# Kernel optimization log

Measured on AMD Instinct MI355X. Metric: run time of the kernel, lower is better.

## Reference

```python
import jax, jax.numpy as jnp
import numpy as np

# Problem sizes (see shape_source)
N_MICRO, E_MICRO = 131072, 1048576
N_MACRO, E_MACRO = 6400, 51200
B, T, NG = 64, 50, 5          # batch graphs, target_seq_len, nodes_per_group
IN_DIM, H, S = 384, 256, 64   # in_dim, hidden_dim, state_dim
NODES_PER_MACRO = 100         # N_MACRO // B


def gcn_conv(x, ei, ew, W, b, num_nodes):
    """PyG-style GCNConv with self-loops: out = D^-1/2 (A+I) D^-1/2 (xW) + b."""
    h = x @ W                                     # [N, H]
    src, dst = ei[0], ei[1]
    deg = jax.ops.segment_sum(ew, dst, num_segments=num_nodes) + 1.0  # +1 self loop
    dinv = jax.lax.rsqrt(deg)
    norm = dinv[src] * ew * dinv[dst]             # [E]
    out = jax.ops.segment_sum(h[src] * norm[:, None], dst, num_segments=num_nodes)
    out = out + h * (dinv * dinv)[:, None]        # self-loop term
    return out + b


def mamba_block(u, W_in, W_dtBC, dt_bias, A_log, Dp, W_out):
    """Mamba2-style selective scan block with gating and residual. u: [B, T, H]."""
    Bb, Tt, Hh = u.shape
    xz = u @ W_in                                  # [B,T,2H]
    x, z = xz[..., :Hh], xz[..., Hh:]
    dbc = u @ W_dtBC                               # [B,T,1+2S]
    n = (dbc.shape[-1] - 1) // 2
    dt = jax.nn.softplus(dbc[..., :1] + dt_bias)   # [B,T,1]
    Bm = dbc[..., 1:1 + n]                         # [B,T,S]
    Cm = dbc[..., 1 + n:]                          # [B,T,S]
    A = -jnp.exp(A_log)                            # [H]
    decay = jnp.exp(dt * A)                        # [B,T,H]
    dx = dt * x                                    # [B,T,H]

    def step(hst, inp):
        dec_t, dx_t, b_t, c_t = inp                # [B,H],[B,H],[B,S],[B,S]
        hst = dec_t[:, :, None] * hst + dx_t[:, :, None] * b_t[:, None, :]
        y_t = jnp.einsum('bhn,bn->bh', hst, c_t)
        return hst, y_t

    h0 = jnp.zeros((Bb, Hh, n), dtype=u.dtype)
    inputs = (decay.transpose(1, 0, 2), dx.transpose(1, 0, 2),
              Bm.transpose(1, 0, 2), Cm.transpose(1, 0, 2))
    _, ys = jax.lax.scan(step, h0, inputs)         # ys: [T,B,H]
    y = ys.transpose(1, 0, 2) + Dp * x
    return (y * jax.nn.silu(z)) @ W_out + u


def setup_inputs() -> dict:
    key = jax.random.key(0)
    ks = jax.random.split(key, 16)
    sc = 0.02
    d = {}
    d['micro_x'] = jax.random.normal(ks[0], (N_MICRO, IN_DIM), jnp.float32)
    d['micro_ew'] = jax.random.uniform(ks[1], (E_MICRO,), jnp.float32)
    d['macro_x'] = jax.random.normal(ks[2], (N_MACRO, IN_DIM), jnp.float32)
    d['macro_ew'] = jax.random.uniform(ks[3], (E_MACRO,), jnp.float32)
    d['Wg_micro'] = jax.random.normal(ks[4], (IN_DIM, H), jnp.float32) * sc
    d['bg_micro'] = jnp.zeros((H,), jnp.float32)
    d['Wg_macro'] = jax.random.normal(ks[5], (IN_DIM, H), jnp.float32) * sc
    d['bg_macro'] = jnp.zeros((H,), jnp.float32)
    d['W_in'] = jax.random.normal(ks[6], (H, 2 * H), jnp.float32) * sc
    d['W_dtBC'] = jax.random.normal(ks[7], (H, 1 + 2 * S), jnp.float32) * sc
    d['dt_bias'] = jnp.zeros((1,), jnp.float32)
    d['A_log'] = jnp.zeros((H,), jnp.float32)
    d['Dp'] = jnp.ones((H,), jnp.float32)
    d['W_out'] = jax.random.normal(ks[8], (H, H), jnp.float32) * sc
    d['W1'] = jax.random.normal(ks[9], (2 * H, H), jnp.float32) * sc
    d['b1'] = jnp.zeros((H,), jnp.float32)
    d['W2'] = jax.random.normal(ks[10], (H, 2 * H), jnp.float32) * sc
    d['b2'] = jnp.zeros((2 * H,), jnp.float32)
    d['micro_ei'] = jax.random.randint(ks[11], (2, E_MICRO), 0, N_MICRO, jnp.int32)
    d['gather_idx'] = jax.random.randint(ks[12], (B, T, NG), 0, N_MICRO, jnp.int32)
    d['mask'] = jnp.ones((B, T), jnp.bool_)
    d['macro_ei'] = jax.random.randint(ks[13], (2, E_MACRO), 0, N_MACRO, jnp.int32)
    return d


def reference(micro_x, micro_ew, macro_x, macro_ew, Wg_micro, bg_micro,
              Wg_macro, bg_macro, W_in, W_dtBC, dt_bias, A_log, Dp, W_out,
              W1, b1, W2, b2, micro_ei, gather_idx, mask, macro_ei):
    # micro branch: per-snapshot GCN over the flattened batched snapshot graph
    gcn_out = gcn_conv(micro_x, micro_ei, micro_ew, Wg_micro, bg_micro, N_MICRO)
    # scatter GCN outputs into padded [B,T,NG,H] embeddings, zero where masked
    emb = gcn_out[gather_idx] * mask[:, :, None, None].astype(gcn_out.dtype)
    seq = emb.mean(axis=2)                          # [B,T,H] mean over node slots
    seq = mamba_block(seq, W_in, W_dtBC, dt_bias, A_log, Dp, W_out)
    micro_pooled = seq[:, -1]                       # [B,H]
    # macro branch: GCN + per-graph mean pooling (fixed nodes per graph)
    macro_feat = gcn_conv(macro_x, macro_ei, macro_ew, Wg_macro, bg_macro, N_MACRO)
    macro_pooled = macro_feat.reshape(B, NODES_PER_MACRO, H).mean(axis=1)
    pooled = jnp.concatenate([macro_pooled, micro_pooled], axis=-1)  # [B,2H]
    return jax.nn.relu(pooled @ W1 + b1) @ W2 + b2   # [B,2H]
```

## Files before the change

### kernel.cpp

```cpp
#include <hip/hip_runtime.h>
#include <hip/hip_bf16.h>
#include <cstdint>

#define NMICRO 131072
#define EMICRO 1048576
#define NMACRO 6400
#define EMACRO 51200
#define BB 64
#define TT 50
#define NGATH 5
#define INDIM 384
#define HDIM 256
#define SDIM 64
#define NPM 100
#define NGIDX (BB*TT*NGATH)
#define NINBC 641

typedef __bf16 bf16x8 __attribute__((ext_vector_type(8)));
typedef float  f32x4  __attribute__((ext_vector_type(4)));

#define WT_E0 (INDIM*HDIM)
#define WT_E1 (WT_E0 + 512*HDIM)
#define WT_E2 (WT_E1 + 129*HDIM)
__global__ __launch_bounds__(256) void k_setup(float* __restrict__ degm, float* __restrict__ dega,
                                               int* __restrict__ slot, int* __restrict__ cntm,
                                               int* __restrict__ cnta, int* __restrict__ counters,
                                               const float* __restrict__ Wg, __bf16* __restrict__ Tg,
                                               const float* __restrict__ Win, const float* __restrict__ Wdbc,
                                               __bf16* __restrict__ Tinbc) {
    int i = blockIdx.x * 256 + threadIdx.x;
    if (i < NMICRO) { degm[i] = 1.0f; slot[i] = -1; }
    if (i < NMACRO) { dega[i] = 1.0f; cnta[i] = 0; }
    if (i < NGIDX)  cntm[i] = 0;
    if (i < 64)     counters[i] = 0;
    if (i < WT_E0) {
        int nn = i / INDIM, kk = i - nn * INDIM;
        Tg[i] = (__bf16)Wg[(size_t)kk * HDIM + nn];
    } else if (i < WT_E1) {
        int j = i - WT_E0;
        int nn = j / HDIM, kk = j - nn * HDIM;
        Tinbc[j] = (__bf16)Win[(size_t)kk * 512 + nn];
    } else if (i < WT_E2) {
        int j = i - WT_E1;
        int nn = j / HDIM, kk = j - nn * HDIM;
        Tinbc[(size_t)512 * HDIM + j] = (__bf16)Wdbc[(size_t)kk * 129 + nn];
    }
}

__global__ void k_slot(const int* __restrict__ gidx, int* __restrict__ slot,
                       int* __restrict__ counter, int* __restrict__ node_of_slot) {
    int i = blockIdx.x * 256 + threadIdx.x;
    if (i >= NGIDX) return;
    int node = gidx[i];
    if (atomicCAS(&slot[node], -1, -2) == -1) {
        int s = atomicAdd(counter, 1);
        node_of_slot[s] = node;
        slot[node] = s;
    }
}

__global__ __launch_bounds__(256) void k_deg_count(const int* __restrict__ mei, const float* __restrict__ mew,
                                                   float* __restrict__ degm, const int* __restrict__ slot,
                                                   int* __restrict__ cntm,
                                                   const int* __restrict__ aei, const float* __restrict__ aew,
                                                   float* __restrict__ dega, int* __restrict__ cnta) {
    int i = blockIdx.x * 256 + threadIdx.x;
    if (i >= EMICRO + EMACRO) return;
    if (i < EMICRO) {
        int dst = mei[EMICRO + i];
        atomicAdd(&degm[dst], mew[i]);
        int s = slot[dst];
        if (s >= 0) atomicAdd(&cntm[s], 1);
    } else {
        int j = i - EMICRO;
        int dst = aei[EMACRO + j];
        atomicAdd(&dega[dst], aew[j]);
        atomicAdd(&cnta[dst], 1);
    }
}

__global__ __launch_bounds__(1024) void k_scan_rsqrt(const int* __restrict__ cm, int* __restrict__ sm, int* __restrict__ um,
                                                     const int* __restrict__ ca, int* __restrict__ sa, int* __restrict__ ua,
                                                     float* __restrict__ degm, float* __restrict__ dega) {
    if (blockIdx.x >= 2) {
        int i = (blockIdx.x - 2) * 1024 + threadIdx.x;
        if (i < NMICRO) degm[i] = rsqrtf(degm[i]);
        else { int j = i - NMICRO; if (j < NMACRO) dega[j] = rsqrtf(dega[j]); }
        return;
    }
    const int* cnt; int* start; int* cursor; int n;
    if (blockIdx.x == 0) { cnt = cm; start = sm; cursor = um; n = NGIDX; }
    else                 { cnt = ca; start = sa; cursor = ua; n = NMACRO; }
    __shared__ int wsum[16];
    __shared__ int carry_s;
    const int tid = threadIdx.x;
    const int lane = tid & 63, wv = tid >> 6;
    if (tid == 0) carry_s = 0;
    __syncthreads();
    for (int base = 0; base < n; base += 1024) {
        int i = base + tid;
        int v = (i < n) ? cnt[i] : 0;
        int x = v;
#pragma unroll
        for (int off = 1; off < 64; off <<= 1) {
            int y = __shfl_up(x, off, 64);
            if (lane >= off) x += y;
        }
        if (lane == 63) wsum[wv] = x;
        __syncthreads();
        int carry = carry_s;
        if (wv == 0) {
            int s = (lane < 16) ? wsum[lane] : 0;
#pragma unroll
            for (int off = 1; off < 16; off <<= 1) {
                int y = __shfl_up(s, off, 64);
                if (lane >= off) s += y;
            }
            if (lane < 16) wsum[lane] = s;
        }
        __syncthreads();
        int woff = (wv == 0) ? 0 : wsum[wv - 1];
        if (i < n) { int e = carry + woff + x - v; start[i] = e; cursor[i] = e; }
        __syncthreads();
        if (tid == 0) carry_s = carry + wsum[15];
    }
}

__global__ __launch_bounds__(256) void k_fillcsr(const int* __restrict__ mei, const float* __restrict__ mew,
                                                 const int* __restrict__ slot, const float* __restrict__ dinvm,
                                                 int* __restrict__ curm, int* __restrict__ csrm_src, float* __restrict__ csrm_nrm,
                                                 const int* __restrict__ aei, const float* __restrict__ aew,
                                                 const float* __restrict__ dinva,
                                                 int* __restrict__ cura, int* __restrict__ csra_src, float* __restrict__ csra_nrm) {
    int i = blockIdx.x * 256 + threadIdx.x;
    if (i >= EMICRO + EMACRO) return;
    if (i < EMICRO) {
        int dst = mei[EMICRO + i];
        int s = slot[dst];
        if (s >= 0) {
            int src = mei[i];
            int p = atomicAdd(&curm[s], 1);
            csrm_src[p] = src;
            csrm_nrm[p] = dinvm[src] * mew[i] * dinvm[dst];
        }
    } else {
        int j = i - EMICRO;
        int dst = aei[EMACRO + j];
        int src = aei[j];
        int p = atomicAdd(&cura[dst], 1);
        csra_src[p] = src;
        csra_nrm[p] = dinva[src] * aew[j] * dinva[dst];
    }
}

__global__ __launch_bounds__(256) void k_agg_both(const int* __restrict__ node_of_slot, const int* __restrict__ nslots,
                                                  const int* __restrict__ startm, const int* __restrict__ cntm,
                                                  const int* __restrict__ csrm_src, const float* __restrict__ csrm_nrm,
                                                  const float* __restrict__ xm, const float* __restrict__ dinvm,
                                                  float* __restrict__ aggm,
                                                  const int* __restrict__ starta, const int* __restrict__ cnta,
                                                  const int* __restrict__ csra_src, const float* __restrict__ csra_nrm,
                                                  const float* __restrict__ xa, const float* __restrict__ dinva,
                                                  float* __restrict__ agga) {
    int gwid = (blockIdx.x * 256 + threadIdx.x) >> 6;
    int lane = threadIdx.x & 63;
    if (gwid < NGIDX) {
        if (gwid >= nslots[0]) return;
        int node = node_of_slot[gwid];
        float di = dinvm[node];
        float sc = di * di;
        const float* xr = xm + (size_t)node * INDIM;
        float4 a0 = ((const float4*)xr)[lane];
        float2 a1 = ((const float2*)(xr + 256))[lane];
        a0.x *= sc; a0.y *= sc; a0.z *= sc; a0.w *= sc; a1.x *= sc; a1.y *= sc;
        int st = startm[gwid], en = st + cntm[gwid];
        for (int e = st; e < en; e++) {
            int src = csrm_src[e]; float nrm = csrm_nrm[e];
            const float* r = xm + (size_t)src * INDIM;
            float4 v0 = ((const float4*)r)[lane];
            float2 v1 = ((const float2*)(r + 256))[lane];
            a0.x += v0.x * nrm; a0.y += v0.y * nrm; a0.z += v0.z * nrm; a0.w += v0.w * nrm;
            a1.x += v1.x * nrm; a1.y += v1.y * nrm;
        }
        float* o = aggm + (size_t)gwid * INDIM;
        ((float4*)o)[lane] = a0;
        ((float2*)(o + 256))[lane] = a1;
    } else {
        int wid = gwid - NGIDX;
        if (wid >= NMACRO) return;
        float di = dinva[wid];
        float sc = di * di;
        const float* xr = xa + (size_t)wid * INDIM;
        float4 a0 = ((const float4*)xr)[lane];
        float2 a1 = ((const float2*)(xr + 256))[lane];
        a0.x *= sc; a0.y *= sc; a0.z *= sc; a0.w *= sc; a1.x *= sc; a1.y *= sc;
        int st = starta[wid], en = st + cnta[wid];
        for (int e = st; e < en; e++) {
            int src = csra_src[e]; float nrm = csra_nrm[e];
            const float* r = xa + (size_t)src * INDIM;
            float4 v0 = ((const float4*)r)[lane];
            float2 v1 = ((const float2*)(r + 256))[lane];
            a0.x += v0.x * nrm; a0.y += v0.y * nrm; a0.z += v0.z * nrm; a0.w += v0.w * nrm;
            a1.x += v1.x * nrm; a1.y += v1.y * nrm;
        }
        float* oo = agga + (size_t)wid * INDIM;
        ((float4*)oo)[lane] = a0;
        ((float2*)(oo + 256))[lane] = a1;
    }
}

__global__ __launch_bounds__(256) void k_seqx_pool(const int* __restrict__ gidx, const int* __restrict__ slot,
                                                   const float* __restrict__ aggm, float* __restrict__ seqx,
                                                   const float* __restrict__ agga, float* __restrict__ pooled) {
    if (blockIdx.x < 800) {
        int wid  = blockIdx.x * 4 + (threadIdx.x >> 6);
        int lane = threadIdx.x & 63;
        float4 a0 = {0.f, 0.f, 0.f, 0.f};
        float2 a1 = {0.f, 0.f};
        for (int g = 0; g < NGATH; g++) {
            int node = gidx[wid * NGATH + g];
            int s = slot[node];
            const float* r = aggm + (size_t)s * INDIM;
            float4 v0 = ((const float4*)r)[lane];
            float2 v1 = ((const float2*)(r + 256))[lane];
            a0.x += v0.x; a0.y += v0.y; a0.z += v0.z; a0.w += v0.w;
            a1.x += v1.x; a1.y += v1.y;
        }
        const float inv = 1.0f / NGATH;
        a0.x *= inv; a0.y *= inv; a0.z *= inv; a0.w *= inv; a1.x *= inv; a1.y *= inv;
        float* o = seqx + (size_t)wid * INDIM;
        ((float4*)o)[lane] = a0;
        ((float2*)(o + 256))[lane] = a1;
    } else {
        int i = (blockIdx.x - 800) * 256 + threadIdx.x;
        if (i >= BB * INDIM) return;
        int g = i / INDIM, c = i - g * INDIM;
        float acc = 0.f;
        const float* p = agga + (size_t)g * NPM * INDIM + c;
        for (int j = 0; j < NPM; j++) acc += p[(size_t)j * INDIM];
        pooled[i] = acc * (1.0f / NPM);
    }
}

__global__ __launch_bounds__(256) void k_gemm(const float* __restrict__ A, const __bf16* __restrict__ Wt,
                                              const float* __restrict__ bias, float* __restrict__ C,
                                              int M, int N, int K) {
    const int tid  = threadIdx.x;
    const int wave = tid >> 6;
    const int lane = tid & 63;
    const int l16  = lane & 15;
    const int quad = lane >> 4;
    const int m0   = blockIdx.x * 64;
    const int n0   = blockIdx.y * 256 + wave * 64;

    f32x4 acc[4][4];
#pragma unroll
    for (int a = 0; a < 4; a++)
#pragma unroll
        for (int b = 0; b < 4; b++) acc[a][b] = (f32x4){0.f, 0.f, 0.f, 0.f};

    const __bf16* wptr[4];
    bool nval[4];
#pragma unroll
    for (int nt = 0; nt < 4; nt++) {
        int n = n0 + nt * 16 + l16;
        nval[nt] = (n < N);
        wptr[nt] = Wt + (size_t)(nval[nt] ? n : 0) * K + quad * 8;
    }
    const float* arow = A + (size_t)(m0 + l16) * K + quad * 8;

    for (int k0 = 0; k0 < K; k0 += 32) {
        bf16x8 afr[4];
#pragma unroll
        for (int mt = 0; mt < 4; mt++) {
            const float* ap = arow + (size_t)(mt * 16) * K + k0;
            float4 f0 = *(const float4*)(ap);
            float4 f1 = *(const float4*)(ap + 4);
            afr[mt][0] = (__bf16)f0.x; afr[mt][1] = (__bf16)f0.y;
            afr[mt][2] = (__bf16)f0.z; afr[mt][3] = (__bf16)f0.w;
            afr[mt][4] = (__bf16)f1.x; afr[mt][5] = (__bf16)f1.y;
            afr[mt][6] = (__bf16)f1.z; afr[mt][7] = (__bf16)f1.w;
        }
#pragma unroll
        for (int nt = 0; nt < 4; nt++) {
            bf16x8 bfr;
            if (nval[nt]) {
                bfr = *(const bf16x8*)(wptr[nt] + k0);
            } else {
#pragma unroll
                for (int j = 0; j < 8; j++) bfr[j] = (__bf16)0.0f;
            }
#pragma unroll
            for (int mt = 0; mt < 4; mt++)
                acc[nt][mt] = __builtin_amdgcn_mfma_f32_16x16x32_bf16(afr[mt], bfr, acc[nt][mt], 0, 0, 0);
        }
    }
#pragma unroll
    for (int nt = 0; nt < 4; nt++) {
        if (!nval[nt]) continue;
        int n = n0 + nt * 16 + l16;
        float bb = bias ? bias[n] : 0.f;
#pragma unroll
        for (int mt = 0; mt < 4; mt++) {
            int mrow = m0 + mt * 16 + quad * 4;
#pragma unroll
            for (int r = 0; r < 4; r++) C[(size_t)(mrow + r) * N + n] = acc[nt][mt][r] + bb;
        }
    }
}

__global__ __launch_bounds__(256) void k_mamba_final(const float* __restrict__ xzdbc,
                                                     const float* __restrict__ dt_bias, const float* __restrict__ A_log,
                                                     const float* __restrict__ Dp, const float* __restrict__ W_out,
                                                     const float* __restrict__ seq,
                                                     const float* __restrict__ pooled_x,
                                                     const float* __restrict__ Wg_macro, const float* __restrict__ bg_macro,
                                                     const float* __restrict__ W1, const float* __restrict__ b1,
                                                     const float* __restrict__ W2, const float* __restrict__ b2,
                                                     float* __restrict__ out) {
    __shared__ float sC[SDIM];
    __shared__ float sdt[TT];
    __shared__ float sS[TT];
    __shared__ float sw[TT];
    __shared__ float spx[INDIM];
    __shared__ float shG[HDIM];
    __shared__ float sp[2 * HDIM];
    __shared__ float sh[HDIM];
    const int b = blockIdx.x;
    const int j = threadIdx.x;
    const float* base = xzdbc + (size_t)b * TT * NINBC;
    const float* row49 = base + (size_t)(TT - 1) * NINBC;

    if (j < SDIM) sC[j] = row49[577 + j];
    for (int i = j; i < INDIM; i += 256) spx[i] = pooled_x[(size_t)b * INDIM + i];
    __syncthreads();

    if (j < TT) {
        const float* row = base + (size_t)j * NINBC;
        float v  = row[512] + dt_bias[0];
        float dt = fmaxf(v, 0.f) + log1pf(expf(-fabsf(v)));
        float dot = 0.f;
#pragma unroll
        for (int n = 0; n < SDIM; n++) dot += row[513 + n] * sC[n];
        sdt[j] = dt;
        sw[j]  = dt * dot;
    }
    __syncthreads();
    if (j < TT) {
        float S = 0.f;
        for (int s = j + 1; s < TT; s++) S += sdt[s];
        sS[j] = S;
    }
    float mp = bg_macro[j];
    for (int k = 0; k < INDIM; k++) mp += spx[k] * Wg_macro[(size_t)k * HDIM + j];
    sp[j] = mp;
    __syncthreads();

    float Ah = -expf(A_log[j]);
    float y = 0.f;
#pragma unroll 5
    for (int t = 0; t < TT; t++) {
        y += sw[t] * __expf(Ah * sS[t]) * base[(size_t)t * NINBC + j];
    }
    float x49 = row49[j];
    float z49 = row49[HDIM + j];
    y += Dp[j] * x49;
    float sil = z49 / (1.f + expf(-z49));
    shG[j] = y * sil;
    __syncthreads();
    float acc = 0.f;
    for (int k = 0; k < HDIM; k++) acc += shG[k] * W_out[(size_t)k * HDIM + j];
    sp[HDIM + j] = acc + seq[(size_t)(b * TT + TT - 1) * HDIM + j];
    __syncthreads();

    float a = b1[j];
    for (int k = 0; k < 2 * HDIM; k++) a += sp[k] * W1[(size_t)k * HDIM + j];
    sh[j] = fmaxf(a, 0.f);
    __syncthreads();
    float a0 = b2[j], a1 = b2[HDIM + j];
    for (int k = 0; k < HDIM; k++) {
        float hv = sh[k];
        a0 += hv * W2[(size_t)k * (2 * HDIM) + j];
        a1 += hv * W2[(size_t)k * (2 * HDIM) + HDIM + j];
    }
    out[(size_t)b * (2 * HDIM) + j]        = a0;
    out[(size_t)b * (2 * HDIM) + HDIM + j] = a1;
}

extern "C" void kernel_launch(void* const* d_in, const int* in_sizes, int n_in,
                              void* d_out, int out_size, void* d_ws, size_t ws_size,
                              hipStream_t stream) {
    const float* micro_x   = (const float*)d_in[0];
    const float* micro_ew  = (const float*)d_in[1];
    const float* macro_x   = (const float*)d_in[2];
    const float* macro_ew  = (const float*)d_in[3];
    const float* Wg_micro  = (const float*)d_in[4];
    const float* bg_micro  = (const float*)d_in[5];
    const float* Wg_macro  = (const float*)d_in[6];
    const float* bg_macro  = (const float*)d_in[7];
    const float* W_in      = (const float*)d_in[8];
    const float* W_dtBC    = (const float*)d_in[9];
    const float* dt_bias   = (const float*)d_in[10];
    const float* A_log     = (const float*)d_in[11];
    const float* Dp        = (const float*)d_in[12];
    const float* W_out     = (const float*)d_in[13];
    const float* W1        = (const float*)d_in[14];
    const float* b1        = (const float*)d_in[15];
    const float* W2        = (const float*)d_in[16];
    const float* b2        = (const float*)d_in[17];
    const int*   micro_ei  = (const int*)d_in[18];
    const int*   gather_idx= (const int*)d_in[19];
    const int*   macro_ei  = (const int*)d_in[21];
    float* out = (float*)d_out;

    char* wsb = (char*)d_ws;
    size_t off = 0;
    auto alloc = [&](size_t bytes) -> void* {
        void* p = wsb + off;
        off = (off + bytes + 255) & ~(size_t)255;
        return p;
    };
    float*  agg_micro    = (float*) alloc((size_t)NGIDX * INDIM * 4);
    float*  agg_macro    = (float*) alloc((size_t)NMACRO * INDIM * 4);
    float*  seq_x        = (float*) alloc((size_t)BB * TT * INDIM * 4);
    float*  pooled_x     = (float*) alloc((size_t)BB * INDIM * 4);
    float*  seq          = (float*) alloc((size_t)BB * TT * HDIM * 4);
    float*  xzdbc        = (float*) alloc((size_t)BB * TT * NINBC * 4);
    float*  deg_micro    = (float*) alloc((size_t)NMICRO * 4);
    float*  deg_macro    = (float*) alloc((size_t)NMACRO * 4);
    int*    slot         = (int*)   alloc((size_t)NMICRO * 4);
    int*    node_of_slot = (int*)   alloc((size_t)NGIDX * 4);
    int*    cntm         = (int*)   alloc((size_t)NGIDX * 4);
    int*    startm       = (int*)   alloc((size_t)NGIDX * 4);
    int*    curm         = (int*)   alloc((size_t)NGIDX * 4);
    int*    cnta         = (int*)   alloc((size_t)NMACRO * 4);
    int*    starta       = (int*)   alloc((size_t)NMACRO * 4);
    int*    cura         = (int*)   alloc((size_t)NMACRO * 4);
    int*    csrm_src     = (int*)   alloc((size_t)EMICRO * 4);
    float*  csrm_nrm     = (float*) alloc((size_t)EMICRO * 4);
    int*    csra_src     = (int*)   alloc((size_t)EMACRO * 4);
    float*  csra_nrm     = (float*) alloc((size_t)EMACRO * 4);
    int*    counters     = (int*)   alloc(256);
    __bf16* Wt_g_micro   = (__bf16*)alloc((size_t)HDIM * INDIM * 2);
    __bf16* Wt_inBC      = (__bf16*)alloc((size_t)NINBC * HDIM * 2);
    (void)ws_size; (void)in_sizes; (void)n_in; (void)out_size;

    k_setup<<<(WT_E2 + 255) / 256, 256, 0, stream>>>(deg_micro, deg_macro, slot, cntm, cnta, counters,
                                                     Wg_micro, Wt_g_micro, W_in, W_dtBC, Wt_inBC);

    k_slot<<<(NGIDX + 255) / 256, 256, 0, stream>>>(gather_idx, slot, &counters[0], node_of_slot);
    k_deg_count<<<(EMICRO + EMACRO + 255) / 256, 256, 0, stream>>>(micro_ei, micro_ew, deg_micro, slot, cntm,
                                                                   macro_ei, macro_ew, deg_macro, cnta);
    k_scan_rsqrt<<<2 + (NMICRO + NMACRO + 1023) / 1024, 1024, 0, stream>>>(cntm, startm, curm,
                                                                           cnta, starta, cura,
                                                                           deg_micro, deg_macro);
    k_fillcsr<<<(EMICRO + EMACRO + 255) / 256, 256, 0, stream>>>(micro_ei, micro_ew, slot, deg_micro,
                                                                 curm, csrm_src, csrm_nrm,
                                                                 macro_ei, macro_ew, deg_macro,
                                                                 cura, csra_src, csra_nrm);

    k_agg_both<<<(NGIDX + NMACRO) / 4, 256, 0, stream>>>(node_of_slot, &counters[0],
                                                         startm, cntm, csrm_src, csrm_nrm,
                                                         micro_x, deg_micro, agg_micro,
                                                         starta, cnta, csra_src, csra_nrm,
                                                         macro_x, deg_macro, agg_macro);
    k_seqx_pool<<<800 + 96, 256, 0, stream>>>(gather_idx, slot, agg_micro, seq_x, agg_macro, pooled_x);

    {
        dim3 g((BB * TT) / 64, 1);
        k_gemm<<<g, 256, 0, stream>>>(seq_x, Wt_g_micro, bg_micro, seq, BB * TT, HDIM, INDIM);
    }
    {
        dim3 g((BB * TT) / 64, (NINBC + 255) / 256);
        k_gemm<<<g, 256, 0, stream>>>(seq, Wt_inBC, nullptr, xzdbc, BB * TT, NINBC, HDIM);
    }

    k_mamba_final<<<BB, 256, 0, stream>>>(xzdbc, dt_bias, A_log, Dp, W_out, seq,
                                          pooled_x, Wg_macro, bg_macro, W1, b1, W2, b2, out);
}
```

Measured before the change: 547.7 us.

## Fuse GCN projection and Mamba input GEMMs, move macro pooling into final kernel

Merges the two back-to-back GEMMs (seq_x·Wg and seq·W_inBC) into one kernel. Each block stages its 64-row A tile in shared memory as bf16, recomputes the first GEMM per column-block, and feeds the result through LDS into the second GEMM. The macro mean-pooling moves into the final Mamba kernel, so the pooled_x buffer and one kernel's worth of work go away. The cost is that the first GEMM is computed three times (once per blockIdx.y), and the per-graph pooling now runs inside 64 final blocks with strided reads.

```diff
diff --git a/kernel.cpp b/kernel.cpp
--- a/kernel.cpp
+++ b/kernel.cpp
@@ -17,6 +17,7 @@
 #define NINBC 641
 
 typedef __bf16 bf16x8 __attribute__((ext_vector_type(8)));
+typedef __bf16 bf16x4 __attribute__((ext_vector_type(4)));
 typedef float  f32x4  __attribute__((ext_vector_type(4)));
 
 #define WT_E0 (INDIM*HDIM)
@@ -209,78 +210,128 @@
     }
 }
 
-__global__ __launch_bounds__(256) void k_seqx_pool(const int* __restrict__ gidx, const int* __restrict__ slot,
-                                                   const float* __restrict__ aggm, float* __restrict__ seqx,
-                                                   const float* __restrict__ agga, float* __restrict__ pooled) {
-    if (blockIdx.x < 800) {
-        int wid  = blockIdx.x * 4 + (threadIdx.x >> 6);
-        int lane = threadIdx.x & 63;
-        float4 a0 = {0.f, 0.f, 0.f, 0.f};
-        float2 a1 = {0.f, 0.f};
-        for (int g = 0; g < NGATH; g++) {
-            int node = gidx[wid * NGATH + g];
-            int s = slot[node];
-            const float* r = aggm + (size_t)s * INDIM;
-            float4 v0 = ((const float4*)r)[lane];
-            float2 v1 = ((const float2*)(r + 256))[lane];
-            a0.x += v0.x; a0.y += v0.y; a0.z += v0.z; a0.w += v0.w;
-            a1.x += v1.x; a1.y += v1.y;
-        }
-        const float inv = 1.0f / NGATH;
-        a0.x *= inv; a0.y *= inv; a0.z *= inv; a0.w *= inv; a1.x *= inv; a1.y *= inv;
-        float* o = seqx + (size_t)wid * INDIM;
-        ((float4*)o)[lane] = a0;
-        ((float2*)(o + 256))[lane] = a1;
-    } else {
-        int i = (blockIdx.x - 800) * 256 + threadIdx.x;
-        if (i >= BB * INDIM) return;
-        int g = i / INDIM, c = i - g * INDIM;
-        float acc = 0.f;
-        const float* p = agga + (size_t)g * NPM * INDIM + c;
-        for (int j = 0; j < NPM; j++) acc += p[(size_t)j * INDIM];
-        pooled[i] = acc * (1.0f / NPM);
-    }
-}
-
-__global__ __launch_bounds__(256) void k_gemm(const float* __restrict__ A, const __bf16* __restrict__ Wt,
-                                              const float* __restrict__ bias, float* __restrict__ C,
-                                              int M, int N, int K) {
+__global__ __launch_bounds__(256) void k_seqx(const int* __restrict__ gidx, const int* __restrict__ slot,
+                                              const float* __restrict__ aggm, float* __restrict__ seqx) {
+    int wid  = blockIdx.x * 4 + (threadIdx.x >> 6);
+    int lane = threadIdx.x & 63;
+    float4 a0 = {0.f, 0.f, 0.f, 0.f};
+    float2 a1 = {0.f, 0.f};
+    for (int g = 0; g < NGATH; g++) {
+        int node = gidx[wid * NGATH + g];
+        int s = slot[node];
+        const float* r = aggm + (size_t)s * INDIM;
+        float4 v0 = ((const float4*)r)[lane];
+        float2 v1 = ((const float2*)(r + 256))[lane];
+        a0.x += v0.x; a0.y += v0.y; a0.z += v0.z; a0.w += v0.w;
+        a1.x += v1.x; a1.y += v1.y;
+    }
+    const float inv = 1.0f / NGATH;
+    a0.x *= inv; a0.y *= inv; a0.z *= inv; a0.w *= inv; a1.x *= inv; a1.y *= inv;
+    float* o = seqx + (size_t)wid * INDIM;
+    ((float4*)o)[lane] = a0;
+    ((float2*)(o + 256))[lane] = a1;
+}
+
+#define KP0 392
+#define KP2 264
+__global__ __launch_bounds__(256) void k_proj(const float* __restrict__ seqx,
+                                              const __bf16* __restrict__ Wg_t,
+                                              const float* __restrict__ bg,
+                                              const __bf16* __restrict__ Winbc_t,
+                                              float* __restrict__ seq,
+                                              float* __restrict__ xzdbc) {
+    __shared__ __align__(16) char smem[64 * KP0 * 2];
+    __bf16* A0 = (__bf16*)smem;
+    __bf16* A2 = (__bf16*)smem;
     const int tid  = threadIdx.x;
     const int wave = tid >> 6;
     const int lane = tid & 63;
     const int l16  = lane & 15;
     const int quad = lane >> 4;
     const int m0   = blockIdx.x * 64;
-    const int n0   = blockIdx.y * 256 + wave * 64;
+
+    for (int idx = tid; idx < 64 * 96; idx += 256) {
+        int r = idx / 96, c4 = idx - r * 96;
+        float4 v = *(const float4*)(seqx + (size_t)(m0 + r) * INDIM + c4 * 4);
+        bf16x4 h = { (__bf16)v.x, (__bf16)v.y, (__bf16)v.z, (__bf16)v.w };
+        *(bf16x4*)(A0 + (size_t)r * KP0 + c4 * 4) = h;
+    }
+    __syncthreads();
 
     f32x4 acc[4][4];
 #pragma unroll
     for (int a = 0; a < 4; a++)
 #pragma unroll
         for (int b = 0; b < 4; b++) acc[a][b] = (f32x4){0.f, 0.f, 0.f, 0.f};
-
+    {
+        const __bf16* wbase = Wg_t + (size_t)(wave * 64 + l16) * INDIM + quad * 8;
+        for (int k0 = 0; k0 < INDIM; k0 += 32) {
+            bf16x8 afr[4];
+#pragma unroll
+            for (int mt = 0; mt < 4; mt++)
+                afr[mt] = *(const bf16x8*)(A0 + (size_t)(mt * 16 + l16) * KP0 + k0 + quad * 8);
+#pragma unroll
+            for (int nt = 0; nt < 4; nt++) {
+                bf16x8 bfr = *(const bf16x8*)(wbase + (size_t)(nt * 16) * INDIM + k0);
+#pragma unroll
+                for (int mt = 0; mt < 4; mt++)
+                    acc[nt][mt] = __builtin_amdgcn_mfma_f32_16x16x32_bf16(afr[mt], bfr, acc[nt][mt], 0, 0, 0);
+            }
+        }
+    }
+#pragma unroll
+    for (int nt = 0; nt < 4; nt++) {
+        int n = wave * 64 + nt * 16 + l16;
+        float bb = bg[n];
+#pragma unroll
+        for (int mt = 0; mt < 4; mt++)
+#pragma unroll
+            for (int r = 0; r < 4; r++) acc[nt][mt][r] += bb;
+    }
+    if (blockIdx.y == 0) {
+#pragma unroll
+        for (int nt = 0; nt < 4; nt++) {
+            int n = wave * 64 + nt * 16 + l16;
+#pragma unroll
+            for (int mt = 0; mt < 4; mt++) {
+                int mrow = mt * 16 + quad * 4;
+#pragma unroll
+                for (int r = 0; r < 4; r++) seq[(size_t)(m0 + mrow + r) * HDIM + n] = acc[nt][mt][r];
+            }
+        }
+    }
+    __syncthreads();
+#pragma unroll
+    for (int nt = 0; nt < 4; nt++) {
+        int n = wave * 64 + nt * 16 + l16;
+#pragma unroll
+        for (int mt = 0; mt < 4; mt++) {
+            int mrow = mt * 16 + quad * 4;
+#pragma unroll
+            for (int r = 0; r < 4; r++) A2[(size_t)(mrow + r) * KP2 + n] = (__bf16)acc[nt][mt][r];
+        }
+    }
+    __syncthreads();
+
+    const int n0c = blockIdx.y * 256 + wave * 64;
+    f32x4 acc2[4][4];
+#pragma unroll
+    for (int a = 0; a < 4; a++)
+#pragma unroll
+        for (int b = 0; b < 4; b++) acc2[a][b] = (f32x4){0.f, 0.f, 0.f, 0.f};
+    bool nval[4];
     const __bf16* wptr[4];
-    bool nval[4];
 #pragma unroll
     for (int nt = 0; nt < 4; nt++) {
-        int n = n0 + nt * 16 + l16;
-        nval[nt] = (n < N);
-        wptr[nt] = Wt + (size_t)(nval[nt] ? n : 0) * K + quad * 8;
-    }
-    const float* arow = A + (size_t)(m0 + l16) * K + quad * 8;
-
-    for (int k0 = 0; k0 < K; k0 += 32) {
+        int n = n0c + nt * 16 + l16;
+        nval[nt] = (n < NINBC);
+        wptr[nt] = Winbc_t + (size_t)(nval[nt] ? n : 0) * HDIM + quad * 8;
+    }
+    for (int k0 = 0; k0 < HDIM; k0 += 32) {
         bf16x8 afr[4];
 #pragma unroll
-        for (int mt = 0; mt < 4; mt++) {
-            const float* ap = arow + (size_t)(mt * 16) * K + k0;
-            float4 f0 = *(const float4*)(ap);
-            float4 f1 = *(const float4*)(ap + 4);
-            afr[mt][0] = (__bf16)f0.x; afr[mt][1] = (__bf16)f0.y;
-            afr[mt][2] = (__bf16)f0.z; afr[mt][3] = (__bf16)f0.w;
-            afr[mt][4] = (__bf16)f1.x; afr[mt][5] = (__bf16)f1.y;
-            afr[mt][6] = (__bf16)f1.z; afr[mt][7] = (__bf16)f1.w;
-        }
+        for (int mt = 0; mt < 4; mt++)
+            afr[mt] = *(const bf16x8*)(A2 + (size_t)(mt * 16 + l16) * KP2 + k0 + quad * 8);
 #pragma unroll
         for (int nt = 0; nt < 4; nt++) {
             bf16x8 bfr;
@@ -292,19 +343,18 @@
             }
 #pragma unroll
             for (int mt = 0; mt < 4; mt++)
-                acc[nt][mt] = __builtin_amdgcn_mfma_f32_16x16x32_bf16(afr[mt], bfr, acc[nt][mt], 0, 0, 0);
+                acc2[nt][mt] = __builtin_amdgcn_mfma_f32_16x16x32_bf16(afr[mt], bfr, acc2[nt][mt], 0, 0, 0);
         }
     }
 #pragma unroll
     for (int nt = 0; nt < 4; nt++) {
         if (!nval[nt]) continue;
-        int n = n0 + nt * 16 + l16;
-        float bb = bias ? bias[n] : 0.f;
+        int n = n0c + nt * 16 + l16;
 #pragma unroll
         for (int mt = 0; mt < 4; mt++) {
-            int mrow = m0 + mt * 16 + quad * 4;
-#pragma unroll
-            for (int r = 0; r < 4; r++) C[(size_t)(mrow + r) * N + n] = acc[nt][mt][r] + bb;
+            int mrow = mt * 16 + quad * 4;
+#pragma unroll
+            for (int r = 0; r < 4; r++) xzdbc[(size_t)(m0 + mrow + r) * NINBC + n] = acc2[nt][mt][r];
         }
     }
 }
@@ -313,7 +363,7 @@
                                                      const float* __restrict__ dt_bias, const float* __restrict__ A_log,
                                                      const float* __restrict__ Dp, const float* __restrict__ W_out,
                                                      const float* __restrict__ seq,
-                                                     const float* __restrict__ pooled_x,
+                                                     const float* __restrict__ agg_macro,
                                                      const float* __restrict__ Wg_macro, const float* __restrict__ bg_macro,
                                                      const float* __restrict__ W1, const float* __restrict__ b1,
                                                      const float* __restrict__ W2, const float* __restrict__ b2,
@@ -332,7 +382,12 @@
     const float* row49 = base + (size_t)(TT - 1) * NINBC;
 
     if (j < SDIM) sC[j] = row49[577 + j];
-    for (int i = j; i < INDIM; i += 256) spx[i] = pooled_x[(size_t)b * INDIM + i];
+    for (int i = j; i < INDIM; i += 256) {
+        float acc = 0.f;
+        const float* p = agg_macro + (size_t)b * NPM * INDIM + i;
+        for (int r = 0; r < NPM; r++) acc += p[(size_t)r * INDIM];
+        spx[i] = acc * (1.0f / NPM);
+    }
     __syncthreads();
 
     if (j < TT) {
@@ -423,7 +478,6 @@
     float*  agg_micro    = (float*) alloc((size_t)NGIDX * INDIM * 4);
     float*  agg_macro    = (float*) alloc((size_t)NMACRO * INDIM * 4);
     float*  seq_x        = (float*) alloc((size_t)BB * TT * INDIM * 4);
-    float*  pooled_x     = (float*) alloc((size_t)BB * INDIM * 4);
     float*  seq          = (float*) alloc((size_t)BB * TT * HDIM * 4);
     float*  xzdbc        = (float*) alloc((size_t)BB * TT * NINBC * 4);
     float*  deg_micro    = (float*) alloc((size_t)NMICRO * 4);
@@ -464,17 +518,13 @@
                                                          micro_x, deg_micro, agg_micro,
                                                          starta, cnta, csra_src, csra_nrm,
                                                          macro_x, deg_macro, agg_macro);
-    k_seqx_pool<<<800 + 96, 256, 0, stream>>>(gather_idx, slot, agg_micro, seq_x, agg_macro, pooled_x);
+    k_seqx<<<800, 256, 0, stream>>>(gather_idx, slot, agg_micro, seq_x);
 
     {
-        dim3 g((BB * TT) / 64, 1);
-        k_gemm<<<g, 256, 0, stream>>>(seq_x, Wt_g_micro, bg_micro, seq, BB * TT, HDIM, INDIM);
-    }
-    {
-        dim3 g((BB * TT) / 64, (NINBC + 255) / 256);
-        k_gemm<<<g, 256, 0, stream>>>(seq, Wt_inBC, nullptr, xzdbc, BB * TT, NINBC, HDIM);
+        dim3 g(50, 3);
+        k_proj<<<g, 256, 0, stream>>>(seq_x, Wt_g_micro, bg_micro, Wt_inBC, seq, xzdbc);
     }
 
     k_mamba_final<<<BB, 256, 0, stream>>>(xzdbc, dt_bias, A_log, Dp, W_out, seq,
-                                          pooled_x, Wg_macro, bg_macro, W1, b1, W2, b2, out);
-}
+                                          agg_macro, Wg_macro, bg_macro, W1, b1, W2, b2, out);
+}
```

Result: no change. 541.5 us (-1.1%).
